# Kernel tuning notes

Hardware: AMD Instinct MI355X
Metric: run time of the kernel (lower is better)

Reference implementation:

```python
import jax, jax.numpy as jnp
import numpy as np

DMODEL = 1024
HEADS = 16
KEY_DIM = DMODEL // HEADS


def setup_inputs() -> dict:
    key = jax.random.key(0)
    k0, k1, k2, k3, k4 = jax.random.split(key, 5)
    scale = 1.0 / np.sqrt(DMODEL)
    return {
        "inputs": jax.random.normal(k0, (2, 2048, DMODEL), dtype=jnp.float32),
        "Wq": jax.random.normal(k1, (DMODEL, DMODEL), dtype=jnp.float32) * scale,
        "Wk": jax.random.normal(k2, (DMODEL, DMODEL), dtype=jnp.float32) * scale,
        "Wv": jax.random.normal(k3, (DMODEL, DMODEL), dtype=jnp.float32) * scale,
        "Wo": jax.random.normal(k4, (DMODEL, DMODEL), dtype=jnp.float32) * scale,
    }


def reference(inputs, Wq, Wk, Wv, Wo):
    B, S, _ = inputs.shape
    # nn.Linear(bias=False): y = x @ W.T ; then reshape to (B, S, H, Dh) and transpose to (B, H, S, Dh)
    def proj(W):
        return (inputs @ W.T).reshape(B, S, HEADS, KEY_DIM).transpose(0, 2, 1, 3)

    q, k, v = proj(Wq), proj(Wk), proj(Wv)
    scale = 1.0 / np.sqrt(KEY_DIM).astype(np.float32)
    score = jnp.einsum('bhsd,bhtd->bhst', q, k) * scale  # [B,H,S,S]
    attn = jax.nn.softmax(score, axis=-1)
    out = jnp.einsum('bhst,bhtd->bhsd', attn, v)  # [B,H,S,Dh]
    out = out.transpose(0, 2, 1, 3).reshape(B, S, HEADS * KEY_DIM)
    return out @ Wo.T
```

## Files before the change

### kernel.cpp

```cpp
#include <hip/hip_runtime.h>
#include <hip/hip_bf16.h>
#include <stdint.h>

typedef __attribute__((ext_vector_type(8))) short short8;
typedef __attribute__((ext_vector_type(4))) float floatx4;

#define MFMA16(a, b, c) __builtin_amdgcn_mfma_f32_16x16x32_bf16((a), (b), (c), 0, 0, 0)

static __device__ __forceinline__ uint16_t f2bf(float f) {
  union { float f; uint32_t u; } x; x.f = f;
  uint32_t r = x.u + 0x7fffu + ((x.u >> 16) & 1u);
  return (uint16_t)(r >> 16);
}

static __device__ __forceinline__ uint32_t cvtpk_bf16(float lo, float hi) {
  uint32_t r;
  asm("v_cvt_pk_bf16_f32 %0, %1, %2" : "=v"(r) : "v"(lo), "v"(hi));
  return r;
}

constexpr int DM = 1024, NH = 16, KD = 64, NB = 2, SQ = 2048;
constexpr int MTOT = NB * SQ;
constexpr int NT = SQ / 64;

__global__ void convert_kernel(const float* __restrict__ X,
                               const float* __restrict__ Wq, const float* __restrict__ Wk,
                               const float* __restrict__ Wv, const float* __restrict__ Wo,
                               uint16_t* __restrict__ Xb, uint16_t* __restrict__ Wqkvb,
                               uint16_t* __restrict__ Wob) {
  const int NX = MTOT * DM;
  const int NW = DM * DM;
  const int TOT8 = (NX + 4 * NW) / 8;
  for (int t = blockIdx.x * blockDim.x + threadIdx.x; t < TOT8; t += gridDim.x * blockDim.x) {
    int i = t * 8;
    const float* src; uint16_t* dst;
    if (i < NX) { src = X + i; dst = Xb + i; }
    else if (i < NX + 3 * NW) {
      int j = i - NX; dst = Wqkvb + j;
      src = (j < NW) ? (Wq + j) : (j < 2 * NW) ? (Wk + (j - NW)) : (Wv + (j - 2 * NW));
    } else {
      int j = i - NX - 3 * NW; src = Wo + j; dst = Wob + j;
    }
    float4 a = ((const float4*)src)[0];
    float4 b = ((const float4*)src)[1];
    ushort4 o0, o1;
    o0.x = f2bf(a.x); o0.y = f2bf(a.y); o0.z = f2bf(a.z); o0.w = f2bf(a.w);
    o1.x = f2bf(b.x); o1.y = f2bf(b.y); o1.z = f2bf(b.z); o1.w = f2bf(b.w);
    ((ushort4*)dst)[0] = o0;
    ((ushort4*)dst)[1] = o1;
  }
}

template <int MODE>
__global__ __launch_bounds__(256) void gemm_bt(const uint16_t* __restrict__ Aq,
                                               const uint16_t* __restrict__ Bq, int Ntiles,
                                               uint16_t* __restrict__ Qb, uint16_t* __restrict__ Kb,
                                               uint16_t* __restrict__ VTb, float* __restrict__ Out) {
  __shared__ uint16_t Al[128 * 32];
  __shared__ uint16_t Bl[128 * 32];
  const int K = 1024;
  int nwg = gridDim.x;
  int bid = (blockIdx.x & 7) * (nwg >> 3) + (blockIdx.x >> 3);
  int bm = bid / Ntiles, bn = bid % Ntiles;
  int brow = bm * 128, bcol = bn * 128;
  int tid = threadIdx.x;
  int w = tid >> 6, lane = tid & 63, g = lane >> 4, c16 = lane & 15;
  int wm = w >> 1, wn = w & 1;
  int rr = tid >> 2;
  int ce = (tid & 3) * 8;

  floatx4 acc[4][4] = {};

  for (int k0 = 0; k0 < K; k0 += 32) {
    __syncthreads();
#pragma unroll
    for (int c = 0; c < 2; ++c) {
      __builtin_amdgcn_global_load_lds(
          (const __attribute__((address_space(1))) void*)(Aq + (size_t)(brow + c * 64 + rr) * K + k0 + ce),
          (__attribute__((address_space(3))) void*)((char*)Al + c * 4096 + w * 1024), 16, 0, 0);
      __builtin_amdgcn_global_load_lds(
          (const __attribute__((address_space(1))) void*)(Bq + (size_t)(bcol + c * 64 + rr) * K + k0 + ce),
          (__attribute__((address_space(3))) void*)((char*)Bl + c * 4096 + w * 1024), 16, 0, 0);
    }
    __syncthreads();
    short8 af[4], bf[4];
#pragma unroll
    for (int mt = 0; mt < 4; ++mt)
      af[mt] = *(const short8*)&Al[(wm * 64 + mt * 16 + c16) * 32 + g * 8];
#pragma unroll
    for (int nt = 0; nt < 4; ++nt)
      bf[nt] = *(const short8*)&Bl[(wn * 64 + nt * 16 + c16) * 32 + g * 8];
#pragma unroll
    for (int mt = 0; mt < 4; ++mt)
#pragma unroll
      for (int nt = 0; nt < 4; ++nt)
        acc[mt][nt] = MFMA16(af[mt], bf[nt], acc[mt][nt]);
  }

#pragma unroll
  for (int mt = 0; mt < 4; ++mt) {
#pragma unroll
    for (int nt = 0; nt < 4; ++nt) {
      int n = bcol + wn * 64 + nt * 16 + c16;
#pragma unroll
      for (int r = 0; r < 4; ++r) {
        int m = brow + wm * 64 + mt * 16 + g * 4 + r;
        float v = acc[mt][nt][r];
        if (MODE == 0) {
          int proj = n >> 10;
          int hd = n & 1023;
          int h = hd >> 6, d = hd & 63;
          int b = m >> 11, s = m & 2047;
          size_t bh = (size_t)(b * NH + h);
          if (proj == 0) {
            Qb[(bh * SQ + s) * KD + d] = f2bf(v * 0.18033688011112042f);
          } else if (proj == 1) {
            int st = s >> 4, r2 = s & 15, k8 = d >> 3, j = d & 7;
            Kb[bh * (size_t)(SQ * KD) + (((size_t)(st * 8 + k8) * 16 + r2) * 8 + j)] = f2bf(v);
          } else {
            int kt = s >> 6, kvl = s & 63;
            int c = kvl >> 5, tth = (kvl >> 4) & 1, gg = (kvl >> 2) & 3, rs = kvl & 3;
            int jp = tth * 4 + rs;
            int dt = d >> 4, cc = d & 15;
            VTb[bh * (size_t)(SQ * KD) + (size_t)kt * 4096 +
                (size_t)((c * 4 + dt) * 512 + gg * 128 + cc * 8 + jp)] = f2bf(v);
          }
        } else {
          Out[(size_t)m * DM + n] = v;
        }
      }
    }
  }
}

__global__ __launch_bounds__(256, 4) void attn_kernel(const uint16_t* __restrict__ Q,
                                                      const uint16_t* __restrict__ Kt,
                                                      const uint16_t* __restrict__ Vt,
                                                      uint16_t* __restrict__ O) {
  int bid = blockIdx.x;
  int bh = bid & 31, qt = bid >> 5;
  int qb = qt * 64;
  int b = bh >> 4, h = bh & 15;
  int tid = threadIdx.x, lane = tid & 63, wv = tid >> 6, g = lane >> 4, c16 = lane & 15;

  const uint16_t* Qh = Q + (size_t)bh * SQ * KD;
  const uint16_t* Kh = Kt + (size_t)bh * SQ * KD;
  const uint16_t* Vh = Vt + (size_t)bh * SQ * KD;

  int qrow = qb + wv * 16 + c16;
  short8 qf0 = *(const short8*)&Qh[(size_t)qrow * KD + g * 8];
  short8 qf1 = *(const short8*)&Qh[(size_t)qrow * KD + 32 + g * 8];

  float l = 0.0f;
  floatx4 accO[4] = {};

  const floatx4 SHIFT_INIT = {-16.0f, -16.0f, -16.0f, -16.0f};

  short8 kf[4][2];
  short8 vf[2][4];

#define LOADK(tile)                                                                 \
  {                                                                                 \
    const uint16_t* kt_ = Kh + (size_t)(tile) * 4096;                               \
    _Pragma("unroll") for (int tt = 0; tt < 4; ++tt)                                \
        _Pragma("unroll") for (int hf = 0; hf < 2; ++hf)                            \
            kf[tt][hf] = *(const short8*)&kt_[tt * 1024 + hf * 512 + lane * 8];     \
  }
#define LOADV(tile)                                                                 \
  {                                                                                 \
    const uint16_t* vt_ = Vh + (size_t)(tile) * 4096;                               \
    _Pragma("unroll") for (int c = 0; c < 2; ++c)                                   \
        _Pragma("unroll") for (int dt = 0; dt < 4; ++dt)                            \
            vf[c][dt] = *(const short8*)&vt_[(c * 4 + dt) * 512 + lane * 8];        \
  }

  LOADK(0);
  LOADV(0);

  for (int t = 0; t < NT; ++t) {
    int tn = (t + 1 < NT) ? (t + 1) : t;

    floatx4 sacc[4];
#pragma unroll
    for (int tt = 0; tt < 4; ++tt) sacc[tt] = SHIFT_INIT;
    __builtin_amdgcn_s_setprio(1);
#pragma unroll
    for (int tt = 0; tt < 4; ++tt) {
      sacc[tt] = MFMA16(kf[tt][0], qf0, sacc[tt]);
      sacc[tt] = MFMA16(kf[tt][1], qf1, sacc[tt]);
    }
    __builtin_amdgcn_s_setprio(0);

    LOADK(tn);

#pragma unroll
    for (int tt = 0; tt < 4; ++tt)
#pragma unroll
      for (int r = 0; r < 4; ++r)
        sacc[tt][r] = exp2f(sacc[tt][r]);
    float s01 = (sacc[0][0] + sacc[0][1]) + (sacc[0][2] + sacc[0][3]);
    float s23 = (sacc[1][0] + sacc[1][1]) + (sacc[1][2] + sacc[1][3]);
    float s45 = (sacc[2][0] + sacc[2][1]) + (sacc[2][2] + sacc[2][3]);
    float s67 = (sacc[3][0] + sacc[3][1]) + (sacc[3][2] + sacc[3][3]);
    l += (s01 + s23) + (s45 + s67);

    union { uint32_t u[4]; short8 s8; } pa[2];
#pragma unroll
    for (int c = 0; c < 2; ++c) {
      pa[c].u[0] = cvtpk_bf16(sacc[2 * c][0], sacc[2 * c][1]);
      pa[c].u[1] = cvtpk_bf16(sacc[2 * c][2], sacc[2 * c][3]);
      pa[c].u[2] = cvtpk_bf16(sacc[2 * c + 1][0], sacc[2 * c + 1][1]);
      pa[c].u[3] = cvtpk_bf16(sacc[2 * c + 1][2], sacc[2 * c + 1][3]);
    }
    __builtin_amdgcn_s_setprio(1);
#pragma unroll
    for (int c = 0; c < 2; ++c)
#pragma unroll
      for (int dt = 0; dt < 4; ++dt)
        accO[dt] = MFMA16(pa[c].s8, vf[c][dt], accO[dt]);
    __builtin_amdgcn_s_setprio(0);

    LOADV(tn);
  }
#undef LOADK
#undef LOADV

  l += __shfl_xor(l, 16);
  l += __shfl_xor(l, 32);

  float lv[4];
#pragma unroll
  for (int r = 0; r < 4; ++r) lv[r] = 1.0f / __shfl(l, g * 4 + r);
#pragma unroll
  for (int dt = 0; dt < 4; ++dt) {
#pragma unroll
    for (int r = 0; r < 4; ++r) {
      int s = qb + wv * 16 + g * 4 + r;
      int d = dt * 16 + c16;
      O[((size_t)(b * SQ + s)) * DM + h * KD + d] = f2bf(accO[dt][r] * lv[r]);
    }
  }
}

extern "C" void kernel_launch(void* const* d_in, const int* in_sizes, int n_in,
                              void* d_out, int out_size, void* d_ws, size_t ws_size,
                              hipStream_t stream) {
  const float* X = (const float*)d_in[0];
  const float* Wq = (const float*)d_in[1];
  const float* Wk = (const float*)d_in[2];
  const float* Wv = (const float*)d_in[3];
  const float* Wo = (const float*)d_in[4];
  float* out = (float*)d_out;

  char* ws = (char*)d_ws;
  uint16_t* Xb    = (uint16_t*)(ws);
  uint16_t* Wqkvb = (uint16_t*)(ws + 8388608);
  uint16_t* Wob   = (uint16_t*)(ws + 14680064);
  uint16_t* Qb    = (uint16_t*)(ws + 16777216);
  uint16_t* Kb    = (uint16_t*)(ws + 25165824);
  uint16_t* VTb   = (uint16_t*)(ws + 33554432);
  uint16_t* Ob    = (uint16_t*)(ws + 41943040);

  hipLaunchKernelGGL(convert_kernel, dim3(1024), dim3(256), 0, stream,
                     X, Wq, Wk, Wv, Wo, Xb, Wqkvb, Wob);
  hipLaunchKernelGGL((gemm_bt<0>), dim3(32 * 24), dim3(256), 0, stream,
                     Xb, Wqkvb, 24, Qb, Kb, VTb, nullptr);
  hipLaunchKernelGGL(attn_kernel, dim3(1024), dim3(256), 0, stream,
                     Qb, Kb, VTb, Ob);
  hipLaunchKernelGGL((gemm_bt<1>), dim3(32 * 8), dim3(256), 0, stream,
                     Ob, Wob, 8, nullptr, nullptr, nullptr, out);
}
```

Measured before the change: 214.9 us.

## Share K/V tiles through LDS across 8 waves and shrink output GEMM tiles

The attention kernel now runs 512-thread blocks covering 128 query rows. K and V tiles are staged cooperatively into double-buffered LDS with global_load_lds, so each tile is fetched from global memory once per block rather than once per wave. This trades per-wave global loads for LDS reads plus one block barrier per tile. The output projection switches to a dedicated 64x128-tile GEMM with 512 workgroups, to fill the CUs better than the previous 256-block launch.

```diff
diff --git a/kernel.cpp b/kernel.cpp
--- a/kernel.cpp
+++ b/kernel.cpp
@@ -51,14 +51,14 @@
   }
 }
 
-template <int MODE>
-__global__ __launch_bounds__(256) void gemm_bt(const uint16_t* __restrict__ Aq,
-                                               const uint16_t* __restrict__ Bq, int Ntiles,
-                                               uint16_t* __restrict__ Qb, uint16_t* __restrict__ Kb,
-                                               uint16_t* __restrict__ VTb, float* __restrict__ Out) {
+__global__ __launch_bounds__(256) void gemm_qkv(const uint16_t* __restrict__ Aq,
+                                                const uint16_t* __restrict__ Bq,
+                                                uint16_t* __restrict__ Qb, uint16_t* __restrict__ Kb,
+                                                uint16_t* __restrict__ VTb) {
   __shared__ uint16_t Al[128 * 32];
   __shared__ uint16_t Bl[128 * 32];
   const int K = 1024;
+  const int Ntiles = 24;
   int nwg = gridDim.x;
   int bid = (blockIdx.x & 7) * (nwg >> 3) + (blockIdx.x >> 3);
   int bm = bid / Ntiles, bn = bid % Ntiles;
@@ -106,40 +106,97 @@
       for (int r = 0; r < 4; ++r) {
         int m = brow + wm * 64 + mt * 16 + g * 4 + r;
         float v = acc[mt][nt][r];
-        if (MODE == 0) {
-          int proj = n >> 10;
-          int hd = n & 1023;
-          int h = hd >> 6, d = hd & 63;
-          int b = m >> 11, s = m & 2047;
-          size_t bh = (size_t)(b * NH + h);
-          if (proj == 0) {
-            Qb[(bh * SQ + s) * KD + d] = f2bf(v * 0.18033688011112042f);
-          } else if (proj == 1) {
-            int st = s >> 4, r2 = s & 15, k8 = d >> 3, j = d & 7;
-            Kb[bh * (size_t)(SQ * KD) + (((size_t)(st * 8 + k8) * 16 + r2) * 8 + j)] = f2bf(v);
-          } else {
-            int kt = s >> 6, kvl = s & 63;
-            int c = kvl >> 5, tth = (kvl >> 4) & 1, gg = (kvl >> 2) & 3, rs = kvl & 3;
-            int jp = tth * 4 + rs;
-            int dt = d >> 4, cc = d & 15;
-            VTb[bh * (size_t)(SQ * KD) + (size_t)kt * 4096 +
-                (size_t)((c * 4 + dt) * 512 + gg * 128 + cc * 8 + jp)] = f2bf(v);
-          }
+        int proj = n >> 10;
+        int hd = n & 1023;
+        int h = hd >> 6, d = hd & 63;
+        int b = m >> 11, s = m & 2047;
+        size_t bh = (size_t)(b * NH + h);
+        if (proj == 0) {
+          Qb[(bh * SQ + s) * KD + d] = f2bf(v * 0.18033688011112042f);
+        } else if (proj == 1) {
+          int st = s >> 4, r2 = s & 15, k8 = d >> 3, j = d & 7;
+          Kb[bh * (size_t)(SQ * KD) + (((size_t)(st * 8 + k8) * 16 + r2) * 8 + j)] = f2bf(v);
         } else {
-          Out[(size_t)m * DM + n] = v;
+          int kt = s >> 6, kvl = s & 63;
+          int c = kvl >> 5, tth = (kvl >> 4) & 1, gg = (kvl >> 2) & 3, rs = kvl & 3;
+          int jp = tth * 4 + rs;
+          int dt = d >> 4, cc = d & 15;
+          VTb[bh * (size_t)(SQ * KD) + (size_t)kt * 4096 +
+              (size_t)((c * 4 + dt) * 512 + gg * 128 + cc * 8 + jp)] = f2bf(v);
         }
       }
     }
   }
 }
 
-__global__ __launch_bounds__(256, 4) void attn_kernel(const uint16_t* __restrict__ Q,
+__global__ __launch_bounds__(256) void gemm_out64(const uint16_t* __restrict__ Aq,
+                                                  const uint16_t* __restrict__ Bq,
+                                                  float* __restrict__ Out) {
+  __shared__ uint16_t Al[64 * 32];
+  __shared__ uint16_t Bl[128 * 32];
+  const int K = 1024;
+  int nwg = gridDim.x;
+  int bid = (blockIdx.x & 7) * (nwg >> 3) + (blockIdx.x >> 3);
+  int bm = bid >> 3, bn = bid & 7;
+  int brow = bm * 64, bcol = bn * 128;
+  int tid = threadIdx.x;
+  int w = tid >> 6, lane = tid & 63, g = lane >> 4, c16 = lane & 15;
+  int wm = w >> 1, wn = w & 1;
+  int rr = tid >> 2;
+  int ce = (tid & 3) * 8;
+
+  floatx4 acc[2][4] = {};
+
+  for (int k0 = 0; k0 < K; k0 += 32) {
+    __syncthreads();
+    __builtin_amdgcn_global_load_lds(
+        (const __attribute__((address_space(1))) void*)(Aq + (size_t)(brow + rr) * K + k0 + ce),
+        (__attribute__((address_space(3))) void*)((char*)Al + w * 1024), 16, 0, 0);
+#pragma unroll
+    for (int c = 0; c < 2; ++c) {
+      __builtin_amdgcn_global_load_lds(
+          (const __attribute__((address_space(1))) void*)(Bq + (size_t)(bcol + c * 64 + rr) * K + k0 + ce),
+          (__attribute__((address_space(3))) void*)((char*)Bl + c * 4096 + w * 1024), 16, 0, 0);
+    }
+    __syncthreads();
+    short8 af[2], bf[4];
+#pragma unroll
+    for (int mt = 0; mt < 2; ++mt)
+      af[mt] = *(const short8*)&Al[(wm * 32 + mt * 16 + c16) * 32 + g * 8];
+#pragma unroll
+    for (int nt = 0; nt < 4; ++nt)
+      bf[nt] = *(const short8*)&Bl[(wn * 64 + nt * 16 + c16) * 32 + g * 8];
+#pragma unroll
+    for (int mt = 0; mt < 2; ++mt)
+#pragma unroll
+      for (int nt = 0; nt < 4; ++nt)
+        acc[mt][nt] = MFMA16(af[mt], bf[nt], acc[mt][nt]);
+  }
+
+#pragma unroll
+  for (int mt = 0; mt < 2; ++mt) {
+#pragma unroll
+    for (int nt = 0; nt < 4; ++nt) {
+      int n = bcol + wn * 64 + nt * 16 + c16;
+#pragma unroll
+      for (int r = 0; r < 4; ++r) {
+        int m = brow + wm * 32 + mt * 16 + g * 4 + r;
+        Out[(size_t)m * DM + n] = acc[mt][nt][r];
+      }
+    }
+  }
+}
+
+__global__ __launch_bounds__(512, 4) void attn_kernel(const uint16_t* __restrict__ Q,
                                                       const uint16_t* __restrict__ Kt,
                                                       const uint16_t* __restrict__ Vt,
                                                       uint16_t* __restrict__ O) {
+  __shared__ __attribute__((aligned(16))) uint16_t Kbuf[2][4096];
+  __shared__ __attribute__((aligned(16))) uint16_t Vbuf[2][4096];
+
   int bid = blockIdx.x;
   int bh = bid & 31, qt = bid >> 5;
-  int qb = qt * 64;
+  int qb = qt * 128;
   int b = bh >> 4, h = bh & 15;
   int tid = threadIdx.x, lane = tid & 63, wv = tid >> 6, g = lane >> 4, c16 = lane & 15;
 
@@ -153,32 +210,38 @@
 
   float l = 0.0f;
   floatx4 accO[4] = {};
-
   const floatx4 SHIFT_INIT = {-16.0f, -16.0f, -16.0f, -16.0f};
 
-  short8 kf[4][2];
-  short8 vf[2][4];
-
-#define LOADK(tile)                                                                 \
-  {                                                                                 \
-    const uint16_t* kt_ = Kh + (size_t)(tile) * 4096;                               \
-    _Pragma("unroll") for (int tt = 0; tt < 4; ++tt)                                \
-        _Pragma("unroll") for (int hf = 0; hf < 2; ++hf)                            \
-            kf[tt][hf] = *(const short8*)&kt_[tt * 1024 + hf * 512 + lane * 8];     \
-  }
-#define LOADV(tile)                                                                 \
-  {                                                                                 \
-    const uint16_t* vt_ = Vh + (size_t)(tile) * 4096;                               \
-    _Pragma("unroll") for (int c = 0; c < 2; ++c)                                   \
-        _Pragma("unroll") for (int dt = 0; dt < 4; ++dt)                            \
-            vf[c][dt] = *(const short8*)&vt_[(c * 4 + dt) * 512 + lane * 8];        \
-  }
-
-  LOADK(0);
-  LOADV(0);
+  auto stage = [&](int buf, int tile) {
+    __builtin_amdgcn_global_load_lds(
+        (const __attribute__((address_space(1))) void*)(Kh + (size_t)tile * 4096 + wv * 512 + lane * 8),
+        (__attribute__((address_space(3))) void*)((char*)&Kbuf[buf][0] + wv * 1024), 16, 0, 0);
+    __builtin_amdgcn_global_load_lds(
+        (const __attribute__((address_space(1))) void*)(Vh + (size_t)tile * 4096 + wv * 512 + lane * 8),
+        (__attribute__((address_space(3))) void*)((char*)&Vbuf[buf][0] + wv * 1024), 16, 0, 0);
+  };
+
+  stage(0, 0);
+  __syncthreads();
 
   for (int t = 0; t < NT; ++t) {
+    int cur = t & 1;
     int tn = (t + 1 < NT) ? (t + 1) : t;
+    stage(cur ^ 1, tn);
+
+    const char* kb = (const char*)&Kbuf[cur][0];
+    const char* vb = (const char*)&Vbuf[cur][0];
+    short8 kf[4][2], vf[2][4];
+#pragma unroll
+    for (int tt = 0; tt < 4; ++tt)
+#pragma unroll
+      for (int hf = 0; hf < 2; ++hf)
+        kf[tt][hf] = *(const short8*)(kb + tt * 2048 + hf * 1024 + lane * 16);
+#pragma unroll
+    for (int c = 0; c < 2; ++c)
+#pragma unroll
+      for (int dt = 0; dt < 4; ++dt)
+        vf[c][dt] = *(const short8*)(vb + (c * 4 + dt) * 1024 + lane * 16);
 
     floatx4 sacc[4];
 #pragma unroll
@@ -190,8 +253,6 @@
       sacc[tt] = MFMA16(kf[tt][1], qf1, sacc[tt]);
     }
     __builtin_amdgcn_s_setprio(0);
-
-    LOADK(tn);
 
 #pragma unroll
     for (int tt = 0; tt < 4; ++tt)
@@ -220,10 +281,8 @@
         accO[dt] = MFMA16(pa[c].s8, vf[c][dt], accO[dt]);
     __builtin_amdgcn_s_setprio(0);
 
-    LOADV(tn);
-  }
-#undef LOADK
-#undef LOADV
+    __syncthreads();
+  }
 
   l += __shfl_xor(l, 16);
   l += __shfl_xor(l, 32);
@@ -263,10 +322,10 @@
 
   hipLaunchKernelGGL(convert_kernel, dim3(1024), dim3(256), 0, stream,
                      X, Wq, Wk, Wv, Wo, Xb, Wqkvb, Wob);
-  hipLaunchKernelGGL((gemm_bt<0>), dim3(32 * 24), dim3(256), 0, stream,
-                     Xb, Wqkvb, 24, Qb, Kb, VTb, nullptr);
-  hipLaunchKernelGGL(attn_kernel, dim3(1024), dim3(256), 0, stream,
+  hipLaunchKernelGGL(gemm_qkv, dim3(32 * 24), dim3(256), 0, stream,
+                     Xb, Wqkvb, Qb, Kb, VTb);
+  hipLaunchKernelGGL(attn_kernel, dim3(512), dim3(512), 0, stream,
                      Qb, Kb, VTb, Ob);
-  hipLaunchKernelGGL((gemm_bt<1>), dim3(32 * 8), dim3(256), 0, stream,
-                     Ob, Wob, 8, nullptr, nullptr, nullptr, out);
-}
+  hipLaunchKernelGGL(gemm_out64, dim3(512), dim3(256), 0, stream,
+                     Ob, Wob, out);
+}
```

After: 194.7 us. 9.4% less time.
